# Kernel tuning notes

Measured on AMD Instinct MI355X. Metric: run time of the kernel, lower is better.

## Reference

```python
import jax, jax.numpy as jnp
import numpy as np

N_ENT = 2000
GAT_EMB = 64
GAT_HID = 3
HIDDEN = 256
BATCH = 8
ALPHA = 0.2  # LeakyReLU negative slope
MASK_FILL = jnp.float32(9e-15)  # original fills masked-out logits with 9e-15 (NOT -inf)


def setup_inputs() -> dict:
    key = jax.random.key(0)
    k1, k2, k3, k4, k5, k6 = jax.random.split(key, 6)
    emb = jax.random.normal(k1, (N_ENT, GAT_EMB), dtype=jnp.float32)
    W = jax.random.normal(k2, (GAT_EMB, GAT_HID), dtype=jnp.float32) * 0.2
    a = jax.random.normal(k3, (2 * GAT_HID, 1), dtype=jnp.float32) * 0.2
    fc1_w = jax.random.normal(k4, (HIDDEN, N_ENT * GAT_HID), dtype=jnp.float32) * 0.02
    fc1_b = jax.random.normal(k5, (HIDDEN,), dtype=jnp.float32) * 0.02
    adj = jax.random.randint(k6, (BATCH, N_ENT, N_ENT), 0, 2, dtype=jnp.int32)
    return {"emb": emb, "W": W, "a": a, "fc1_w": fc1_w, "fc1_b": fc1_b, "adj": adj}


def reference(emb, W, a, fc1_w, fc1_b, adj):
    # h = emb @ W : [N, 3] -- shared across all graphs in the batch
    h = emb @ W
    # Pairwise logits: original concatenates [h_i, h_j] and dots with a;
    # equivalent to (h @ a1)_i + (h @ a2)_j via broadcasting (no O(N^2*2H) tensor).
    s1 = h @ a[:GAT_HID, 0]   # [N]
    s2 = h @ a[GAT_HID:, 0]   # [N]
    e = jax.nn.leaky_relu(s1[:, None] + s2[None, :], negative_slope=ALPHA)  # [N, N]
    # Mask by adjacency (fill 9e-15, matching original), softmax over neighbors (dim=1)
    masked = jnp.where(adj > 0, e[None, :, :], MASK_FILL)  # [B, N, N]
    att = jax.nn.softmax(masked, axis=2)
    # Weighted aggregation + ELU (concat=True head)
    h_prime = jnp.einsum('bij,jd->bid', att, h)  # [B, N, 3]
    x = jax.nn.elu(h_prime).reshape(att.shape[0], -1)  # [B, N*3]
    return x @ fc1_w.T + fc1_b  # [B, hidden]
```

## Files before the change

kernel.cpp:

```cpp
#include <hip/hip_runtime.h>
#include <cstddef>

#define N_ENT   2000
#define GAT_EMB 64
#define HIDDEN  256
#define BATCH   8
#define ALPHA   0.2f

typedef _Float16 half4 __attribute__((ext_vector_type(4)));

#define WS_HX_OFF      8192
#define WS_HY_OFF      12288
#define WS_HZ_OFF      16384
#define WS_S1_OFF      20480
#define WS_TABLE_BYTES 28672
#define WS_X_OFF       28672
#define WS_TIER2_BYTES 124672

__global__ __launch_bounds__(256) void k_init(const float* __restrict__ fc1_b,
                                              float* __restrict__ out) {
    int idx = blockIdx.x * 256 + threadIdx.x;
    out[idx] = fc1_b[idx & (HIDDEN - 1)];
}

__global__ __launch_bounds__(256) void k_prep(const float* __restrict__ emb,
                                              const float* __restrict__ W,
                                              const float* __restrict__ a,
                                              float* __restrict__ ws) {
    __shared__ float sW[GAT_EMB * 3];
    __shared__ float sa[6];
    int t = threadIdx.x;
    if (t < GAT_EMB * 3) sW[t] = W[t];
    if (t < 6)           sa[t] = a[t];
    __syncthreads();
    int i = blockIdx.x * 256 + t;
    if (i >= N_ENT) return;
    const float4* er = (const float4*)(emb + (size_t)i * GAT_EMB);
    float h0 = 0.f, h1 = 0.f, h2 = 0.f;
#pragma unroll
    for (int k4 = 0; k4 < GAT_EMB / 4; ++k4) {
        float4 e4 = er[k4];
        int k = 4 * k4;
        h0 += e4.x * sW[(k + 0) * 3 + 0]; h1 += e4.x * sW[(k + 0) * 3 + 1]; h2 += e4.x * sW[(k + 0) * 3 + 2];
        h0 += e4.y * sW[(k + 1) * 3 + 0]; h1 += e4.y * sW[(k + 1) * 3 + 1]; h2 += e4.y * sW[(k + 1) * 3 + 2];
        h0 += e4.z * sW[(k + 2) * 3 + 0]; h1 += e4.z * sW[(k + 2) * 3 + 1]; h2 += e4.z * sW[(k + 2) * 3 + 2];
        h0 += e4.w * sW[(k + 3) * 3 + 0]; h1 += e4.w * sW[(k + 3) * 3 + 1]; h2 += e4.w * sW[(k + 3) * 3 + 2];
    }
    ws[i] = h0 * sa[3] + h1 * sa[4] + h2 * sa[5];
    ((_Float16*)((char*)ws + WS_HX_OFF))[i] = (_Float16)h0;
    ((_Float16*)((char*)ws + WS_HY_OFF))[i] = (_Float16)h1;
    ((_Float16*)((char*)ws + WS_HZ_OFF))[i] = (_Float16)h2;
    ws[WS_S1_OFF / 4 + i] = h0 * sa[0] + h1 * sa[1] + h2 * sa[2];
}

__global__ __launch_bounds__(256, 5) void k_main(const float* __restrict__ emb,
                                                 const float* __restrict__ W,
                                                 const float* __restrict__ a,
                                                 const float* __restrict__ fc1_w,
                                                 const int*   __restrict__ adj,
                                                 float* __restrict__ wsf,
                                                 int mode,
                                                 float* __restrict__ out) {
    __shared__ __align__(16) unsigned char smem[20480];
    float*    s2s = (float*)smem;
    _Float16* hxs = (_Float16*)(smem + 8192);
    _Float16* hys = (_Float16*)(smem + 12288);
    _Float16* hzs = (_Float16*)(smem + 16384);
    __shared__ float sW[GAT_EMB * 3];
    __shared__ float sa[6];
    __shared__ float s1sh[1];
    __shared__ float xblk[BATCH][4];

    int t = threadIdx.x;
    int g = blockIdx.x;

    if (mode != 0) {
        const uint4* src = (const uint4*)wsf;
        uint4* dst = (uint4*)smem;
#pragma unroll
        for (int rep = 0; rep < 5; ++rep) dst[rep * 256 + t] = src[rep * 256 + t];
    } else {
        if (t < GAT_EMB * 3) sW[t] = W[t];
        if (t < 6)           sa[t] = a[t];
        __syncthreads();
        for (int j = t; j < N_ENT; j += 256) {
            const float4* er = (const float4*)(emb + (size_t)j * GAT_EMB);
            float h0 = 0.f, h1 = 0.f, h2 = 0.f;
#pragma unroll
            for (int k4 = 0; k4 < GAT_EMB / 4; ++k4) {
                float4 e4 = er[k4];
                int k = 4 * k4;
                h0 += e4.x * sW[(k + 0) * 3 + 0]; h1 += e4.x * sW[(k + 0) * 3 + 1]; h2 += e4.x * sW[(k + 0) * 3 + 2];
                h0 += e4.y * sW[(k + 1) * 3 + 0]; h1 += e4.y * sW[(k + 1) * 3 + 1]; h2 += e4.y * sW[(k + 1) * 3 + 2];
                h0 += e4.z * sW[(k + 2) * 3 + 0]; h1 += e4.z * sW[(k + 2) * 3 + 1]; h2 += e4.z * sW[(k + 2) * 3 + 2];
                h0 += e4.w * sW[(k + 3) * 3 + 0]; h1 += e4.w * sW[(k + 3) * 3 + 1]; h2 += e4.w * sW[(k + 3) * 3 + 2];
            }
            s2s[j] = h0 * sa[3] + h1 * sa[4] + h2 * sa[5];
            hxs[j] = (_Float16)h0; hys[j] = (_Float16)h1; hzs[j] = (_Float16)h2;
            if (j == g) s1sh[0] = h0 * sa[0] + h1 * sa[1] + h2 * sa[2];
        }
    }
    if (t < 2048 - N_ENT) {
        int j = N_ENT + t;
        s2s[j] = 0.f; hxs[j] = (_Float16)0; hys[j] = (_Float16)0; hzs[j] = (_Float16)0;
    }
    __syncthreads();

    int lane = t & 63;
    int w    = t >> 6;
    float s1v = (mode == 0) ? s1sh[0] : wsf[WS_S1_OFF / 4 + g];
    const int* __restrict__ baseA = adj + ((size_t)(2 * w + 0) * N_ENT + g) * N_ENT;
    const int* __restrict__ baseB = adj + ((size_t)(2 * w + 1) * N_ENT + g) * N_ENT;
    int phase = (g + 3 * w) & 7;
    int l4 = lane << 2;

    float aA0 = 0.f, aA1 = 0.f, aA2 = 0.f, aA3 = 0.f;
    float aB0 = 0.f, aB1 = 0.f, aB2 = 0.f, aB3 = 0.f;

#pragma unroll
    for (int s = 0; s < 8; ++s) {
        int c  = (s + phase) & 7;
        int j0 = c * 256 + l4;
        bool valid = (j0 < N_ENT);
        int jc = valid ? j0 : 0;
        int4 mA = *(const int4*)(baseA + jc);
        int4 mB = *(const int4*)(baseB + jc);
        float4 s2v = *(const float4*)&s2s[j0];
        half4  hxv = *(const half4*)&hxs[j0];
        half4  hyv = *(const half4*)&hys[j0];
        half4  hzv = *(const half4*)&hzs[j0];
        float vw = valid ? 1.0f : 0.0f;
        float ev[4], hx[4], hy[4], hz[4];
#pragma unroll
        for (int q = 0; q < 4; ++q) {
            float e = s1v + ((const float*)&s2v)[q];
            ev[q] = __expf(fmaxf(e, 0.f) + ALPHA * fminf(e, 0.f)) ;
            hx[q] = (float)hxv[q]; hy[q] = (float)hyv[q]; hz[q] = (float)hzv[q];
        }
        const int* ma = (const int*)&mA;
        const int* mb = (const int*)&mB;
#pragma unroll
        for (int q = 0; q < 4; ++q) {
            float eA = ((ma[q] > 0) ? ev[q] : 1.0f) * vw;
            aA0 += eA; aA1 += eA * hx[q]; aA2 += eA * hy[q]; aA3 += eA * hz[q];
            float eB = ((mb[q] > 0) ? ev[q] : 1.0f) * vw;
            aB0 += eB; aB1 += eB * hx[q]; aB2 += eB * hy[q]; aB3 += eB * hz[q];
        }
    }

#pragma unroll
    for (int off = 32; off > 0; off >>= 1) {
        aA0 += __shfl_xor(aA0, off, 64); aA1 += __shfl_xor(aA1, off, 64);
        aA2 += __shfl_xor(aA2, off, 64); aA3 += __shfl_xor(aA3, off, 64);
        aB0 += __shfl_xor(aB0, off, 64); aB1 += __shfl_xor(aB1, off, 64);
        aB2 += __shfl_xor(aB2, off, 64); aB3 += __shfl_xor(aB3, off, 64);
    }
    if (lane == 0) {
        float inv = 1.f / aA0;
        float p0 = aA1 * inv, p1 = aA2 * inv, p2 = aA3 * inv;
        xblk[2 * w + 0][0] = (p0 > 0.f) ? p0 : expm1f(p0);
        xblk[2 * w + 0][1] = (p1 > 0.f) ? p1 : expm1f(p1);
        xblk[2 * w + 0][2] = (p2 > 0.f) ? p2 : expm1f(p2);
        inv = 1.f / aB0;
        p0 = aB1 * inv; p1 = aB2 * inv; p2 = aB3 * inv;
        xblk[2 * w + 1][0] = (p0 > 0.f) ? p0 : expm1f(p0);
        xblk[2 * w + 1][1] = (p1 > 0.f) ? p1 : expm1f(p1);
        xblk[2 * w + 1][2] = (p2 > 0.f) ? p2 : expm1f(p2);
    }
    __syncthreads();

    if (mode == 2) {
        if (t < 24) {
            int b = t & 7, c = t >> 3;
            _Float16* x16 = (_Float16*)((char*)wsf + WS_X_OFF);
            x16[(size_t)(3 * g + c) * 8 + b] = (_Float16)xblk[b][c];
        }
    } else {
        int k = (t + g * 19) & 255;
        const float* wr = fc1_w + (size_t)k * (N_ENT * 3) + 3 * g;
        float w0 = wr[0], w1 = wr[1], w2 = wr[2];
#pragma unroll
        for (int b = 0; b < BATCH; ++b) {
            float d = xblk[b][0] * w0 + xblk[b][1] * w1 + xblk[b][2] * w2;
            atomicAdd(&out[b * HIDDEN + k], d);
        }
    }
}

__global__ __launch_bounds__(256) void k_fc(const _Float16* __restrict__ x16,
                                            const float* __restrict__ fc1_w,
                                            const float* __restrict__ fc1_b,
                                            float* __restrict__ out) {
    __shared__ float red[4][8];
    int t = threadIdx.x, lane = t & 63, w = t >> 6;
    int k = blockIdx.x;
    const float* __restrict__ wr = fc1_w + (size_t)k * (N_ENT * 3);
    float acc[BATCH];
#pragma unroll
    for (int b = 0; b < BATCH; ++b) acc[b] = 0.f;
#pragma unroll
    for (int it = 0; it < 6; ++it) {
        int m0 = 4 * t + 1024 * it;
        if (m0 + 3 < N_ENT * 3) {
            float4 wv4 = *(const float4*)(wr + m0);
#pragma unroll
            for (int q = 0; q < 4; ++q) {
                half4 xa = *(const half4*)(x16 + (size_t)(m0 + q) * 8);
                half4 xb = *(const half4*)(x16 + (size_t)(m0 + q) * 8 + 4);
                float wv = ((const float*)&wv4)[q];
                acc[0] += wv * (float)xa[0]; acc[1] += wv * (float)xa[1];
                acc[2] += wv * (float)xa[2]; acc[3] += wv * (float)xa[3];
                acc[4] += wv * (float)xb[0]; acc[5] += wv * (float)xb[1];
                acc[6] += wv * (float)xb[2]; acc[7] += wv * (float)xb[3];
            }
        }
    }
#pragma unroll
    for (int off = 32; off > 0; off >>= 1)
#pragma unroll
        for (int b = 0; b < BATCH; ++b) acc[b] += __shfl_xor(acc[b], off, 64);
    if (lane == 0)
#pragma unroll
        for (int b = 0; b < BATCH; ++b) red[w][b] = acc[b];
    __syncthreads();
    if (t < 8) {
        float s = red[0][t] + red[1][t] + red[2][t] + red[3][t] + fc1_b[k];
        out[t * HIDDEN + k] = s;
    }
}

extern "C" void kernel_launch(void* const* d_in, const int* in_sizes, int n_in,
                              void* d_out, int out_size, void* d_ws, size_t ws_size,
                              hipStream_t stream) {
    const float* emb   = (const float*)d_in[0];
    const float* W     = (const float*)d_in[1];
    const float* a     = (const float*)d_in[2];
    const float* fc1_w = (const float*)d_in[3];
    const float* fc1_b = (const float*)d_in[4];
    const int*   adj   = (const int*)d_in[5];
    float* out = (float*)d_out;
    float* ws  = (float*)d_ws;
    (void)in_sizes; (void)n_in; (void)out_size;

    int tier = (ws_size >= (size_t)WS_TIER2_BYTES) ? 2
             : (ws_size >= (size_t)WS_TABLE_BYTES) ? 1 : 0;

    if (tier < 2)  k_init<<<8, 256, 0, stream>>>(fc1_b, out);
    if (tier >= 1) k_prep<<<8, 256, 0, stream>>>(emb, W, a, ws);
    k_main<<<N_ENT, 256, 0, stream>>>(emb, W, a, fc1_w, adj, ws, tier, out);
    if (tier == 2)
        k_fc<<<HIDDEN, 256, 0, stream>>>((const _Float16*)((char*)d_ws + WS_X_OFF),
                                         fc1_w, fc1_b, out);
}
```

Baseline: 215.2 us.

## Remap k_main blocks to 16 consecutive rows of one batch graph

Each block now handles 16 adjacent rows (4 per wave) from one batch's adjacency instead of one row across all 8 batches, and the grid is halved to 1000 blocks. This cuts the per-block cost of loading the shared h/s2 table, since each block now does twice the attention work per table fill. It drops the rotating phase offset and the masking multiply on full chunks. It recomputes exp per row rather than sharing it across batches, which adds about twice the transcendental work per element.

```diff
diff --git a/kernel.cpp b/kernel.cpp
--- a/kernel.cpp
+++ b/kernel.cpp
@@ -68,17 +68,20 @@
     _Float16* hzs = (_Float16*)(smem + 16384);
     __shared__ float sW[GAT_EMB * 3];
     __shared__ float sa[6];
-    __shared__ float s1sh[1];
-    __shared__ float xblk[BATCH][4];
+    __shared__ float s1sh[16];
+    __shared__ float xblk[48];
 
     int t = threadIdx.x;
-    int g = blockIdx.x;
+    int R0 = blockIdx.x * 16;
+    int b  = R0 / N_ENT;
+    int i_base = R0 - b * N_ENT;
 
     if (mode != 0) {
         const uint4* src = (const uint4*)wsf;
         uint4* dst = (uint4*)smem;
 #pragma unroll
         for (int rep = 0; rep < 5; ++rep) dst[rep * 256 + t] = src[rep * 256 + t];
+        if (t < 16) s1sh[t] = wsf[WS_S1_OFF / 4 + i_base + t];
     } else {
         if (t < GAT_EMB * 3) sW[t] = W[t];
         if (t < 6)           sa[t] = a[t];
@@ -97,7 +100,8 @@
             }
             s2s[j] = h0 * sa[3] + h1 * sa[4] + h2 * sa[5];
             hxs[j] = (_Float16)h0; hys[j] = (_Float16)h1; hzs[j] = (_Float16)h2;
-            if (j == g) s1sh[0] = h0 * sa[0] + h1 * sa[1] + h2 * sa[2];
+            if (j >= i_base && j < i_base + 16)
+                s1sh[j - i_base] = h0 * sa[0] + h1 * sa[1] + h2 * sa[2];
         }
     }
     if (t < 2048 - N_ENT) {
@@ -108,82 +112,100 @@
 
     int lane = t & 63;
     int w    = t >> 6;
-    float s1v = (mode == 0) ? s1sh[0] : wsf[WS_S1_OFF / 4 + g];
-    const int* __restrict__ baseA = adj + ((size_t)(2 * w + 0) * N_ENT + g) * N_ENT;
-    const int* __restrict__ baseB = adj + ((size_t)(2 * w + 1) * N_ENT + g) * N_ENT;
-    int phase = (g + 3 * w) & 7;
+    float s1r[4];
+    const int* __restrict__ rowp[4];
+#pragma unroll
+    for (int r = 0; r < 4; ++r) {
+        s1r[r] = s1sh[4 * w + r];
+        rowp[r] = adj + ((size_t)b * N_ENT + (i_base + 4 * w + r)) * N_ENT;
+    }
+
+    float acc[4][4];
+#pragma unroll
+    for (int r = 0; r < 4; ++r) { acc[r][0] = 0.f; acc[r][1] = 0.f; acc[r][2] = 0.f; acc[r][3] = 0.f; }
+
     int l4 = lane << 2;
-
-    float aA0 = 0.f, aA1 = 0.f, aA2 = 0.f, aA3 = 0.f;
-    float aB0 = 0.f, aB1 = 0.f, aB2 = 0.f, aB3 = 0.f;
-
-#pragma unroll
-    for (int s = 0; s < 8; ++s) {
-        int c  = (s + phase) & 7;
+#pragma unroll
+    for (int c = 0; c < 8; ++c) {
         int j0 = c * 256 + l4;
-        bool valid = (j0 < N_ENT);
+        bool chunk_full = (c != 7);
+        bool valid = chunk_full | (j0 < N_ENT);
         int jc = valid ? j0 : 0;
-        int4 mA = *(const int4*)(baseA + jc);
-        int4 mB = *(const int4*)(baseB + jc);
+
+        int4 m0 = *(const int4*)(rowp[0] + jc);
+        int4 m1 = *(const int4*)(rowp[1] + jc);
+        int4 m2 = *(const int4*)(rowp[2] + jc);
+        int4 m3 = *(const int4*)(rowp[3] + jc);
+
         float4 s2v = *(const float4*)&s2s[j0];
         half4  hxv = *(const half4*)&hxs[j0];
         half4  hyv = *(const half4*)&hys[j0];
         half4  hzv = *(const half4*)&hzs[j0];
+        float hx[4], hy[4], hz[4];
+#pragma unroll
+        for (int q = 0; q < 4; ++q) { hx[q] = (float)hxv[q]; hy[q] = (float)hyv[q]; hz[q] = (float)hzv[q]; }
+
+        const int* mm[4] = { (const int*)&m0, (const int*)&m1, (const int*)&m2, (const int*)&m3 };
         float vw = valid ? 1.0f : 0.0f;
-        float ev[4], hx[4], hy[4], hz[4];
-#pragma unroll
-        for (int q = 0; q < 4; ++q) {
-            float e = s1v + ((const float*)&s2v)[q];
-            ev[q] = __expf(fmaxf(e, 0.f) + ALPHA * fminf(e, 0.f)) ;
-            hx[q] = (float)hxv[q]; hy[q] = (float)hyv[q]; hz[q] = (float)hzv[q];
-        }
-        const int* ma = (const int*)&mA;
-        const int* mb = (const int*)&mB;
-#pragma unroll
-        for (int q = 0; q < 4; ++q) {
-            float eA = ((ma[q] > 0) ? ev[q] : 1.0f) * vw;
-            aA0 += eA; aA1 += eA * hx[q]; aA2 += eA * hy[q]; aA3 += eA * hz[q];
-            float eB = ((mb[q] > 0) ? ev[q] : 1.0f) * vw;
-            aB0 += eB; aB1 += eB * hx[q]; aB2 += eB * hy[q]; aB3 += eB * hz[q];
-        }
-    }
-
-#pragma unroll
-    for (int off = 32; off > 0; off >>= 1) {
-        aA0 += __shfl_xor(aA0, off, 64); aA1 += __shfl_xor(aA1, off, 64);
-        aA2 += __shfl_xor(aA2, off, 64); aA3 += __shfl_xor(aA3, off, 64);
-        aB0 += __shfl_xor(aB0, off, 64); aB1 += __shfl_xor(aB1, off, 64);
-        aB2 += __shfl_xor(aB2, off, 64); aB3 += __shfl_xor(aB3, off, 64);
-    }
+#pragma unroll
+        for (int r = 0; r < 4; ++r) {
+#pragma unroll
+            for (int q = 0; q < 4; ++q) {
+                float e  = s1r[r] + ((const float*)&s2v)[q];
+                float ev = __expf(fmaxf(e, 0.f) + ALPHA * fminf(e, 0.f));
+                float contrib = (mm[r][q] > 0) ? ev : 1.0f;
+                if (!chunk_full) contrib *= vw;
+                acc[r][0] += contrib;
+                acc[r][1] += contrib * hx[q];
+                acc[r][2] += contrib * hy[q];
+                acc[r][3] += contrib * hz[q];
+            }
+        }
+    }
+
+#pragma unroll
+    for (int off = 32; off > 0; off >>= 1)
+#pragma unroll
+        for (int r = 0; r < 4; ++r) {
+            acc[r][0] += __shfl_xor(acc[r][0], off, 64);
+            acc[r][1] += __shfl_xor(acc[r][1], off, 64);
+            acc[r][2] += __shfl_xor(acc[r][2], off, 64);
+            acc[r][3] += __shfl_xor(acc[r][3], off, 64);
+        }
+
     if (lane == 0) {
-        float inv = 1.f / aA0;
-        float p0 = aA1 * inv, p1 = aA2 * inv, p2 = aA3 * inv;
-        xblk[2 * w + 0][0] = (p0 > 0.f) ? p0 : expm1f(p0);
-        xblk[2 * w + 0][1] = (p1 > 0.f) ? p1 : expm1f(p1);
-        xblk[2 * w + 0][2] = (p2 > 0.f) ? p2 : expm1f(p2);
-        inv = 1.f / aB0;
-        p0 = aB1 * inv; p1 = aB2 * inv; p2 = aB3 * inv;
-        xblk[2 * w + 1][0] = (p0 > 0.f) ? p0 : expm1f(p0);
-        xblk[2 * w + 1][1] = (p1 > 0.f) ? p1 : expm1f(p1);
-        xblk[2 * w + 1][2] = (p2 > 0.f) ? p2 : expm1f(p2);
-    }
-    __syncthreads();
-
-    if (mode == 2) {
-        if (t < 24) {
-            int b = t & 7, c = t >> 3;
-            _Float16* x16 = (_Float16*)((char*)wsf + WS_X_OFF);
-            x16[(size_t)(3 * g + c) * 8 + b] = (_Float16)xblk[b][c];
-        }
-    } else {
-        int k = (t + g * 19) & 255;
-        const float* wr = fc1_w + (size_t)k * (N_ENT * 3) + 3 * g;
-        float w0 = wr[0], w1 = wr[1], w2 = wr[2];
-#pragma unroll
-        for (int b = 0; b < BATCH; ++b) {
-            float d = xblk[b][0] * w0 + xblk[b][1] * w1 + xblk[b][2] * w2;
-            atomicAdd(&out[b * HIDDEN + k], d);
-        }
+#pragma unroll
+        for (int r = 0; r < 4; ++r) {
+            float inv = 1.f / acc[r][0];
+            float p0 = acc[r][1] * inv, p1 = acc[r][2] * inv, p2 = acc[r][3] * inv;
+            p0 = (p0 > 0.f) ? p0 : expm1f(p0);
+            p1 = (p1 > 0.f) ? p1 : expm1f(p1);
+            p2 = (p2 > 0.f) ? p2 : expm1f(p2);
+            int c = 3 * (4 * w + r);
+            if (mode == 2) {
+                _Float16* x16 = (_Float16*)((char*)wsf + WS_X_OFF);
+                int i = i_base + 4 * w + r;
+                x16[(size_t)(3 * i + 0) * 8 + b] = (_Float16)p0;
+                x16[(size_t)(3 * i + 1) * 8 + b] = (_Float16)p1;
+                x16[(size_t)(3 * i + 2) * 8 + b] = (_Float16)p2;
+            } else {
+                xblk[c + 0] = p0; xblk[c + 1] = p1; xblk[c + 2] = p2;
+            }
+        }
+    }
+
+    if (mode != 2) {
+        __syncthreads();
+        int k = (t + R0) & 255;
+        const float* wr = fc1_w + (size_t)k * (N_ENT * 3) + 3 * i_base;
+        float d = 0.f;
+#pragma unroll
+        for (int c4 = 0; c4 < 12; ++c4) {
+            float4 wv = *(const float4*)(wr + 4 * c4);
+            d += xblk[4 * c4 + 0] * wv.x + xblk[4 * c4 + 1] * wv.y
+               + xblk[4 * c4 + 2] * wv.z + xblk[4 * c4 + 3] * wv.w;
+        }
+        atomicAdd(&out[b * HIDDEN + k], d);
     }
 }
 
@@ -223,10 +245,8 @@
 #pragma unroll
         for (int b = 0; b < BATCH; ++b) red[w][b] = acc[b];
     __syncthreads();
-    if (t < 8) {
-        float s = red[0][t] + red[1][t] + red[2][t] + red[3][t] + fc1_b[k];
-        out[t * HIDDEN + k] = s;
-    }
+    if (t < 8)
+        out[t * HIDDEN + k] = red[0][t] + red[1][t] + red[2][t] + red[3][t] + fc1_b[k];
 }
 
 extern "C" void kernel_launch(void* const* d_in, const int* in_sizes, int n_in,
@@ -247,7 +267,7 @@
 
     if (tier < 2)  k_init<<<8, 256, 0, stream>>>(fc1_b, out);
     if (tier >= 1) k_prep<<<8, 256, 0, stream>>>(emb, W, a, ws);
-    k_main<<<N_ENT, 256, 0, stream>>>(emb, W, a, fc1_w, adj, ws, tier, out);
+    k_main<<<1000, 256, 0, stream>>>(emb, W, a, fc1_w, adj, ws, tier, out);
     if (tier == 2)
         k_fc<<<HIDDEN, 256, 0, stream>>>((const _Float16*)((char*)d_ws + WS_X_OFF),
                                          fc1_w, fc1_b, out);
```

Result: no change. 214.8 us (-0.2%).
